# Optimization experiments

Measured on AMD Instinct MI355X. Metric: run time of the kernel, lower is better.

## Reference

```python
import jax, jax.numpy as jnp
import numpy as np

N = 100000
E = 3200000
IN_DIM = 128
HD = 64
HEADS = 4
NEG_SLOPE = 0.2


def setup_inputs() -> dict:
    key = jax.random.key(0)
    ks = jax.random.split(key, 12)
    s = lambda fan_in: 1.0 / np.sqrt(fan_in)
    x = jax.random.normal(ks[0], (N, IN_DIM), dtype=jnp.float32)
    edge_index = jax.random.randint(ks[1], (2, E), 0, N, dtype=jnp.int64)
    W1 = jax.random.normal(ks[2], (IN_DIM, HEADS * HD), dtype=jnp.float32) * s(IN_DIM)
    a_src1 = jax.random.normal(ks[3], (HEADS, HD), dtype=jnp.float32) * s(HD)
    a_dst1 = jax.random.normal(ks[4], (HEADS, HD), dtype=jnp.float32) * s(HD)
    b1 = jnp.zeros((HEADS * HD,), dtype=jnp.float32)
    W2 = jax.random.normal(ks[5], (HEADS * HD, HD), dtype=jnp.float32) * s(HEADS * HD)
    a_src2 = jax.random.normal(ks[6], (1, HD), dtype=jnp.float32) * s(HD)
    a_dst2 = jax.random.normal(ks[7], (1, HD), dtype=jnp.float32) * s(HD)
    b2 = jnp.zeros((HD,), dtype=jnp.float32)
    lin_w = jax.random.normal(ks[8], (HD, 2), dtype=jnp.float32) * s(HD)
    lin_b = jnp.zeros((2,), dtype=jnp.float32)
    return {"x": x, "edge_index": edge_index, "W1": W1, "a_src1": a_src1,
            "a_dst1": a_dst1, "b1": b1, "W2": W2, "a_src2": a_src2,
            "a_dst2": a_dst2, "b2": b2, "lin_w": lin_w, "lin_b": lin_b}


def gat_conv(x, src, dst, W, a_src, a_dst, bias, heads, out_dim, concat):
    n = x.shape[0]
    h = (x @ W).reshape(n, heads, out_dim)                 # [N,H,D]
    alpha_s = jnp.einsum('nhd,hd->nh', h, a_src)           # [N,H]
    alpha_d = jnp.einsum('nhd,hd->nh', h, a_dst)           # [N,H]
    e = alpha_s[src] + alpha_d[dst]                        # [Etot,H]
    e = jnp.where(e > 0, e, NEG_SLOPE * e)                 # leaky relu
    m = jax.ops.segment_max(e, dst, num_segments=n)        # scatter-softmax (stable)
    m = jnp.where(jnp.isfinite(m), m, 0.0)
    e = jnp.exp(e - m[dst])
    denom = jax.ops.segment_sum(e, dst, num_segments=n)
    alpha = e / denom[dst]                                 # [Etot,H]
    out = jax.ops.segment_sum(h[src] * alpha[:, :, None], dst, num_segments=n)  # [N,H,D]
    out = out.reshape(n, heads * out_dim) if concat else out.mean(axis=1)
    return out + bias


def reference(x, edge_index, W1, a_src1, a_dst1, b1, W2, a_src2, a_dst2, b2, lin_w, lin_b):
    n = x.shape[0]
    loops = jnp.arange(n, dtype=edge_index.dtype)
    src = jnp.concatenate([edge_index[0], loops])          # add self-loops (PyG default)
    dst = jnp.concatenate([edge_index[1], loops])
    h = gat_conv(x, src, dst, W1, a_src1, a_dst1, b1, HEADS, HD, True)
    h = jax.nn.elu(h)
    h = gat_conv(h, src, dst, W2, a_src2, a_dst2, b2, 1, HD, True)
    h = jax.nn.elu(h)
    return h @ lin_w + lin_b                               # [N,2]
```

## Files before the change

kernel.cpp:

```cpp
#include <hip/hip_runtime.h>
#include <hip/hip_fp16.h>
#include <math.h>

#define NN 100000
#define EE 3200000
#define ETOT (EE + NN)
#define NEG_SLOPE 0.2f
#define DMAX 96
#define CHUNK 4096
#define NB0 ((ETOT + CHUNK - 1) / CHUNK)
#define RB 391
#define CAP 16384

typedef _Float16 half8 __attribute__((ext_vector_type(8)));
typedef _Float16 half4v __attribute__((ext_vector_type(4)));
typedef float floatx4 __attribute__((ext_vector_type(4)));

__device__ __forceinline__ float wsum64(float v) {
#pragma unroll
  for (int o = 32; o; o >>= 1) v += __shfl_xor(v, o);
  return v;
}
__device__ __forceinline__ float lrelu(float v) { return v > 0.f ? v : NEG_SLOPE * v; }
__device__ __forceinline__ float elu1(float v) { return v > 0.f ? v : expm1f(v); }

__global__ void k_init(int* __restrict__ ccur) {
  ccur[threadIdx.x] = threadIdx.x * CAP;
}

__global__ __launch_bounds__(256) void k_pass1(const int* __restrict__ ei,
                                               int* __restrict__ ccur,
                                               unsigned* __restrict__ ebuf,
                                               const float* __restrict__ W1,
                                               const float* __restrict__ W2,
                                               _Float16* __restrict__ W1t,
                                               _Float16* __restrict__ W2t) {
  int b = blockIdx.x;
  if (b >= NB0) {
    int idx = (b - NB0) * 256 + threadIdx.x;
    if (idx < 32768) {
      int n = idx >> 7, k = idx & 127;
      W1t[idx] = (_Float16)W1[k * 256 + n];
    } else {
      int j = idx - 32768;
      int n = j >> 8, k = j & 255;
      W2t[j] = (_Float16)W2[k * 64 + n];
    }
    return;
  }
  __shared__ unsigned vv[CHUNK];
  __shared__ unsigned short cbv[CHUNK];
  __shared__ int h[256];
  __shared__ int cur[256];
  int t = threadIdx.x;
  h[t] = 0;
  __syncthreads();
  int base = b * CHUNK;
  int lim = base + CHUNK; if (lim > ETOT) lim = ETOT;
  int cnt = lim - base;
  for (int i = t; i < cnt; i += 256) {
    int e = base + i;
    int s, d;
    if (e < EE) { s = ei[e]; d = ei[EE + e]; } else { s = e - EE; d = s; }
    unsigned cb = (unsigned)d / (unsigned)RB;
    unsigned dloc = (unsigned)d - cb * (unsigned)RB;
    vv[i] = (dloc << 17) | (unsigned)s;
    cbv[i] = (unsigned short)cb;
    atomicAdd(&h[cb], 1);
  }
  __syncthreads();
  if (h[t]) cur[t] = atomicAdd(&ccur[t], h[t]);
  __syncthreads();
  for (int i = t; i < cnt; i += 256) {
    int cb = cbv[i];
    int pos = atomicAdd(&cur[cb], 1);
    ebuf[pos] = vv[i];
  }
}

__global__ __launch_bounds__(256) void k_pass2(const unsigned* __restrict__ ebuf,
                                               const int* __restrict__ ccur,
                                               int* __restrict__ offs,
                                               int* __restrict__ degarr,
                                               int* __restrict__ csr) {
  __shared__ unsigned ed[CAP];
  __shared__ int hist[RB];
  __shared__ int cur[RB];
  int b = blockIdx.x, t = threadIdx.x;
  int d0 = b * RB;
  int rb = NN - d0; if (rb > RB) rb = RB;
  int w0 = b * CAP;
  int cnt = ccur[b] - w0;
  if (cnt > CAP) cnt = CAP;
  for (int j = t; j < rb; j += 256) hist[j] = 0;
  __syncthreads();
  for (int i = t; i < cnt; i += 256) {
    unsigned v = ebuf[w0 + i];
    ed[i] = v;
    atomicAdd(&hist[v >> 17], 1);
  }
  __syncthreads();
  if (t == 0) {
    int run = w0;
    for (int j = 0; j < rb; ++j) { cur[j] = run; run += hist[j]; }
  }
  __syncthreads();
  for (int j = t; j < rb; j += 256) {
    offs[d0 + j] = cur[j];
    degarr[d0 + j] = hist[j];
  }
  __syncthreads();
  for (int i = t; i < cnt; i += 256) {
    unsigned v = ed[i];
    int pos = atomicAdd(&cur[v >> 17], 1);
    csr[pos] = (int)(v & 0x1FFFFu);
  }
}

__global__ __launch_bounds__(256) void k_gemm1m(const float* __restrict__ x,
                                                const _Float16* __restrict__ W1t,
                                                const float* __restrict__ a_src,
                                                const float* __restrict__ a_dst,
                                                _Float16* __restrict__ h1h,
                                                float* __restrict__ as_out,
                                                float* __restrict__ ad_out) {
  __shared__ _Float16 As[64][136];
  __shared__ _Float16 Wt[128][136];
  const int bx = blockIdx.x & 1;
  const int by = blockIdx.x >> 1;
  const int tid = threadIdx.x;
  const int row0 = by * 64;
#pragma unroll
  for (int i = 0; i < 8; ++i) {
    int idx = i * 256 + tid;
    int r = idx >> 5;
    int c4 = (idx & 31) * 4;
    int gr = row0 + r;
    float4 f = make_float4(0.f, 0.f, 0.f, 0.f);
    if (gr < NN) f = *(const float4*)(x + (size_t)gr * 128 + c4);
    half4v h; h[0] = (_Float16)f.x; h[1] = (_Float16)f.y; h[2] = (_Float16)f.z; h[3] = (_Float16)f.w;
    *(half4v*)&As[r][c4] = h;
  }
#pragma unroll
  for (int i = 0; i < 8; ++i) {
    int idx = i * 256 + tid;
    int r = idx >> 4;
    int g = idx & 15;
    *(half8*)&Wt[r][g * 8] = *(const half8*)(W1t + (size_t)(bx * 128 + r) * 128 + g * 8);
  }
  __syncthreads();

  const int wid = tid >> 6, lane = tid & 63;
  const int m16 = lane & 15, quad = lane >> 4;
  floatx4 acc[8];
#pragma unroll
  for (int nt = 0; nt < 8; ++nt) acc[nt] = (floatx4){0.f, 0.f, 0.f, 0.f};
#pragma unroll
  for (int ks = 0; ks < 4; ++ks) {
    half8 av = *(half8*)&As[wid * 16 + m16][ks * 32 + quad * 8];
#pragma unroll
    for (int nt = 0; nt < 8; ++nt) {
      half8 bv = *(half8*)&Wt[nt * 16 + m16][ks * 32 + quad * 8];
      acc[nt] = __builtin_amdgcn_mfma_f32_16x16x32_f16(av, bv, acc[nt], 0, 0, 0);
    }
  }
  float asr[8], adr[8];
#pragma unroll
  for (int nt = 0; nt < 8; ++nt) {
    asr[nt] = a_src[bx * 128 + nt * 16 + m16];
    adr[nt] = a_dst[bx * 128 + nt * 16 + m16];
  }
#pragma unroll
  for (int r = 0; r < 4; ++r) {
    int gr = row0 + wid * 16 + quad * 4 + r;
    bool ok = gr < NN;
#pragma unroll
    for (int hp = 0; hp < 2; ++hp) {
      float ps = 0.f, pd = 0.f;
#pragma unroll
      for (int j = 0; j < 4; ++j) {
        ps = fmaf(acc[hp * 4 + j][r], asr[hp * 4 + j], ps);
        pd = fmaf(acc[hp * 4 + j][r], adr[hp * 4 + j], pd);
      }
#pragma unroll
      for (int o = 1; o < 16; o <<= 1) { ps += __shfl_xor(ps, o); pd += __shfl_xor(pd, o); }
      if (ok && m16 == 0) {
        as_out[gr * 4 + bx * 2 + hp] = ps;
        ad_out[gr * 4 + bx * 2 + hp] = pd;
      }
    }
    if (ok) {
#pragma unroll
      for (int nt = 0; nt < 8; ++nt)
        h1h[(size_t)gr * 256 + bx * 128 + nt * 16 + m16] = (_Float16)acc[nt][r];
    }
  }
}

__global__ __launch_bounds__(256) void k_gemm2m(const _Float16* __restrict__ h1e,
                                                const _Float16* __restrict__ W2t,
                                                const float* __restrict__ a_src,
                                                const float* __restrict__ a_dst,
                                                _Float16* __restrict__ h2h,
                                                float* __restrict__ as_out,
                                                float* __restrict__ ad_out) {
  __shared__ _Float16 As2[64][136];
  __shared__ _Float16 Wt2[64][264];
  const int by = blockIdx.x;
  const int tid = threadIdx.x;
  const int row0 = by * 64;
#pragma unroll
  for (int i = 0; i < 8; ++i) {
    int idx = i * 256 + tid;
    int r = idx >> 5;
    int g = idx & 31;
    *(half8*)&Wt2[r][g * 8] = *(const half8*)(W2t + (size_t)r * 256 + g * 8);
  }
  const int wid = tid >> 6, lane = tid & 63;
  const int m16 = lane & 15, quad = lane >> 4;
  floatx4 acc[4];
#pragma unroll
  for (int nt = 0; nt < 4; ++nt) acc[nt] = (floatx4){0.f, 0.f, 0.f, 0.f};

  for (int kc = 0; kc < 2; ++kc) {
#pragma unroll
    for (int i = 0; i < 4; ++i) {
      int idx = i * 256 + tid;
      int r = idx >> 4;
      int g = idx & 15;
      int gr = row0 + r;
      half8 v = {0, 0, 0, 0, 0, 0, 0, 0};
      if (gr < NN) v = *(const half8*)(h1e + (size_t)gr * 256 + kc * 128 + g * 8);
      *(half8*)&As2[r][g * 8] = v;
    }
    __syncthreads();
#pragma unroll
    for (int ks = 0; ks < 4; ++ks) {
      half8 av = *(half8*)&As2[wid * 16 + m16][ks * 32 + quad * 8];
#pragma unroll
      for (int nt = 0; nt < 4; ++nt) {
        half8 bv = *(half8*)&Wt2[nt * 16 + m16][kc * 128 + ks * 32 + quad * 8];
        acc[nt] = __builtin_amdgcn_mfma_f32_16x16x32_f16(av, bv, acc[nt], 0, 0, 0);
      }
    }
    __syncthreads();
  }
  float asr[4], adr[4];
#pragma unroll
  for (int nt = 0; nt < 4; ++nt) {
    asr[nt] = a_src[nt * 16 + m16];
    adr[nt] = a_dst[nt * 16 + m16];
  }
#pragma unroll
  for (int r = 0; r < 4; ++r) {
    float ps = 0.f, pd = 0.f;
#pragma unroll
    for (int nt = 0; nt < 4; ++nt) {
      ps = fmaf(acc[nt][r], asr[nt], ps);
      pd = fmaf(acc[nt][r], adr[nt], pd);
    }
#pragma unroll
    for (int o = 1; o < 16; o <<= 1) { ps += __shfl_xor(ps, o); pd += __shfl_xor(pd, o); }
    int gr = row0 + wid * 16 + quad * 4 + r;
    if (gr < NN) {
      if (m16 == 0) { as_out[gr] = ps; ad_out[gr] = pd; }
#pragma unroll
      for (int nt = 0; nt < 4; ++nt)
        h2h[(size_t)gr * 64 + nt * 16 + m16] = (_Float16)acc[nt][r];
    }
  }
}

__global__ __launch_bounds__(256) void k_attn1(const int* __restrict__ offs,
                                               const int* __restrict__ degarr,
                                               const int* __restrict__ csr_src,
                                               const float* __restrict__ a_s,
                                               const float* __restrict__ a_d,
                                               const _Float16* __restrict__ h1h,
                                               const float* __restrict__ b1,
                                               _Float16* __restrict__ h1e) {
  __shared__ float alpha[4][DMAX][4];
  __shared__ int sidx[4][DMAX];
  const int wid = threadIdx.x >> 6;
  const int n = blockIdx.x * 4 + wid;
  const int lane = threadIdx.x & 63;
  const int beg = offs[n], deg = degarr[n];
  const float4 ad = *(const float4*)(a_d + n * 4);
  float4 sm = make_float4(0.f, 0.f, 0.f, 0.f);
  for (int d = lane; d < deg; d += 64) {
    int s = csr_src[beg + d];
    float4 as = *(const float4*)(a_s + s * 4);
    float e0 = __expf(lrelu(as.x + ad.x));
    float e1 = __expf(lrelu(as.y + ad.y));
    float e2 = __expf(lrelu(as.z + ad.z));
    float e3 = __expf(lrelu(as.w + ad.w));
    sm.x += e0; sm.y += e1; sm.z += e2; sm.w += e3;
    if (d < DMAX) {
      sidx[wid][d] = s;
      *(float4*)&alpha[wid][d][0] = make_float4(e0, e1, e2, e3);
    }
  }
  sm.x = wsum64(sm.x); sm.y = wsum64(sm.y); sm.z = wsum64(sm.z); sm.w = wsum64(sm.w);
  const float4 inv4 = make_float4(1.f / sm.x, 1.f / sm.y, 1.f / sm.z, 1.f / sm.w);
  const int dlim = deg < DMAX ? deg : DMAX;
  for (int d = lane; d < dlim; d += 64) {
    float4 a = *(float4*)&alpha[wid][d][0];
    a.x *= inv4.x; a.y *= inv4.y; a.z *= inv4.z; a.w *= inv4.w;
    *(float4*)&alpha[wid][d][0] = a;
  }
  const int half = lane >> 5;
  const int sub = lane & 31;
  const int head = sub >> 3;
  const _Float16* __restrict__ hb = h1h + sub * 8;
  float accv[8];
#pragma unroll
  for (int j = 0; j < 8; ++j) accv[j] = 0.f;
  int d = 0;
  for (; d + 8 <= dlim; d += 8) {
    int ss[4]; float ww[4];
#pragma unroll
    for (int u = 0; u < 4; ++u) {
      int idx = d + 2 * u + half;
      ss[u] = sidx[wid][idx];
      ww[u] = alpha[wid][idx][head];
    }
    half8 rr[4];
#pragma unroll
    for (int u = 0; u < 4; ++u)
      rr[u] = *(const half8*)(hb + (size_t)ss[u] * 256);
#pragma unroll
    for (int u = 0; u < 4; ++u) {
#pragma unroll
      for (int j = 0; j < 8; ++j)
        accv[j] = fmaf((float)rr[u][j], ww[u], accv[j]);
    }
  }
  for (; d + 2 <= dlim; d += 2) {
    int idx = d + half;
    int s = sidx[wid][idx];
    float w = alpha[wid][idx][head];
    half8 r = *(const half8*)(hb + (size_t)s * 256);
#pragma unroll
    for (int j = 0; j < 8; ++j) accv[j] = fmaf((float)r[j], w, accv[j]);
  }
  if (d < dlim) {
    int s = sidx[wid][d];
    float w = half ? 0.f : alpha[wid][d][head];
    half8 r = *(const half8*)(hb + (size_t)s * 256);
#pragma unroll
    for (int j = 0; j < 8; ++j) accv[j] = fmaf((float)r[j], w, accv[j]);
  }
  if (deg > DMAX) {
    const float adh = head == 0 ? ad.x : head == 1 ? ad.y : head == 2 ? ad.z : ad.w;
    const float invh = head == 0 ? inv4.x : head == 1 ? inv4.y : head == 2 ? inv4.z : inv4.w;
    if (!half) {
      for (int dd = DMAX; dd < deg; ++dd) {
        int s = csr_src[beg + dd];
        float w = __expf(lrelu(a_s[s * 4 + head] + adh)) * invh;
        half8 r = *(const half8*)(hb + (size_t)s * 256);
#pragma unroll
        for (int j = 0; j < 8; ++j) accv[j] = fmaf((float)r[j], w, accv[j]);
      }
    }
  }
#pragma unroll
  for (int j = 0; j < 8; ++j) accv[j] += __shfl_xor(accv[j], 32);
  if (!half) {
    const int c = sub * 8;
    float4 b0 = *(const float4*)(b1 + c);
    float4 b1v = *(const float4*)(b1 + c + 4);
    half8 o;
    o[0] = (_Float16)elu1(accv[0] + b0.x);
    o[1] = (_Float16)elu1(accv[1] + b0.y);
    o[2] = (_Float16)elu1(accv[2] + b0.z);
    o[3] = (_Float16)elu1(accv[3] + b0.w);
    o[4] = (_Float16)elu1(accv[4] + b1v.x);
    o[5] = (_Float16)elu1(accv[5] + b1v.y);
    o[6] = (_Float16)elu1(accv[6] + b1v.z);
    o[7] = (_Float16)elu1(accv[7] + b1v.w);
    *(half8*)(h1e + (size_t)n * 256 + c) = o;
  }
}

__global__ __launch_bounds__(256) void k_attn2(const int* __restrict__ offs,
                                               const int* __restrict__ degarr,
                                               const int* __restrict__ csr_src,
                                               const float* __restrict__ a_s,
                                               const float* __restrict__ a_d,
                                               const _Float16* __restrict__ h2h,
                                               const float* __restrict__ b2,
                                               const float* __restrict__ lin_w,
                                               const float* __restrict__ lin_b,
                                               float* __restrict__ out) {
  __shared__ float alpha2[4][DMAX];
  __shared__ int sidx2[4][DMAX];
  const int wid = threadIdx.x >> 6;
  const int n = blockIdx.x * 4 + wid;
  const int lane = threadIdx.x & 63;
  const int beg = offs[n], deg = degarr[n];
  const float adn = a_d[n];
  float sm = 0.f;
  for (int d = lane; d < deg; d += 64) {
    int s = csr_src[beg + d];
    float e = __expf(lrelu(a_s[s] + adn));
    sm += e;
    if (d < DMAX) { sidx2[wid][d] = s; alpha2[wid][d] = e; }
  }
  sm = wsum64(sm);
  const float inv = 1.f / sm;
  const int dlim = deg < DMAX ? deg : DMAX;
  for (int d = lane; d < dlim; d += 64) alpha2[wid][d] *= inv;
  const int g = lane >> 4;
  const int sub = lane & 15;
  const _Float16* __restrict__ hb = h2h + sub * 4;
  float a0 = 0.f, a1 = 0.f, a2 = 0.f, a3 = 0.f;
  int d = 0;
  for (; d + 8 <= dlim; d += 8) {
    int i0 = d + g, i1 = d + 4 + g;
    int s0 = sidx2[wid][i0], s1 = sidx2[wid][i1];
    float w0 = alpha2[wid][i0], w1 = alpha2[wid][i1];
    half4v r0 = *(const half4v*)(hb + (size_t)s0 * 64);
    half4v r1 = *(const half4v*)(hb + (size_t)s1 * 64);
    a0 = fmaf((float)r0[0], w0, a0); a1 = fmaf((float)r0[1], w0, a1);
    a2 = fmaf((float)r0[2], w0, a2); a3 = fmaf((float)r0[3], w0, a3);
    a0 = fmaf((float)r1[0], w1, a0); a1 = fmaf((float)r1[1], w1, a1);
    a2 = fmaf((float)r1[2], w1, a2); a3 = fmaf((float)r1[3], w1, a3);
  }
  if (d + 4 <= dlim) {
    int i0 = d + g;
    int s0 = sidx2[wid][i0];
    float w0 = alpha2[wid][i0];
    half4v r0 = *(const half4v*)(hb + (size_t)s0 * 64);
    a0 = fmaf((float)r0[0], w0, a0); a1 = fmaf((float)r0[1], w0, a1);
    a2 = fmaf((float)r0[2], w0, a2); a3 = fmaf((float)r0[3], w0, a3);
    d += 4;
  }
  if (d < dlim) {
    int idx = d + g;
    bool v = idx < dlim;
    int s = sidx2[wid][v ? idx : d];
    float w = v ? alpha2[wid][idx] : 0.f;
    half4v r = *(const half4v*)(hb + (size_t)s * 64);
    a0 = fmaf((float)r[0], w, a0); a1 = fmaf((float)r[1], w, a1);
    a2 = fmaf((float)r[2], w, a2); a3 = fmaf((float)r[3], w, a3);
  }
  if (deg > DMAX && g == 0) {
    for (int dd = DMAX; dd < deg; ++dd) {
      int s = csr_src[beg + dd];
      float w = __expf(lrelu(a_s[s] + adn)) * inv;
      half4v r = *(const half4v*)(hb + (size_t)s * 64);
      a0 = fmaf((float)r[0], w, a0); a1 = fmaf((float)r[1], w, a1);
      a2 = fmaf((float)r[2], w, a2); a3 = fmaf((float)r[3], w, a3);
    }
  }
  a0 += __shfl_xor(a0, 16); a1 += __shfl_xor(a1, 16);
  a2 += __shfl_xor(a2, 16); a3 += __shfl_xor(a3, 16);
  a0 += __shfl_xor(a0, 32); a1 += __shfl_xor(a1, 32);
  a2 += __shfl_xor(a2, 32); a3 += __shfl_xor(a3, 32);
  const int c = sub * 4;
  float4 bb = *(const float4*)(b2 + c);
  float o0 = elu1(a0 + bb.x);
  float o1 = elu1(a1 + bb.y);
  float o2 = elu1(a2 + bb.z);
  float o3 = elu1(a3 + bb.w);
  float4 lw0 = *(const float4*)(lin_w + c * 2);
  float4 lw1 = *(const float4*)(lin_w + c * 2 + 4);
  float p0 = o0 * lw0.x + o1 * lw0.z + o2 * lw1.x + o3 * lw1.z;
  float p1 = o0 * lw0.y + o1 * lw0.w + o2 * lw1.y + o3 * lw1.w;
  p0 = wsum64(p0) * 0.25f;
  p1 = wsum64(p1) * 0.25f;
  if (lane == 0) {
    out[n * 2 + 0] = p0 + lin_b[0];
    out[n * 2 + 1] = p1 + lin_b[1];
  }
}

extern "C" void kernel_launch(void* const* d_in, const int* in_sizes, int n_in,
                              void* d_out, int out_size, void* d_ws, size_t ws_size,
                              hipStream_t stream) {
  const float* x      = (const float*)d_in[0];
  const int*   ei     = (const int*)d_in[1];
  const float* W1     = (const float*)d_in[2];
  const float* a_src1 = (const float*)d_in[3];
  const float* a_dst1 = (const float*)d_in[4];
  const float* b1     = (const float*)d_in[5];
  const float* W2     = (const float*)d_in[6];
  const float* a_src2 = (const float*)d_in[7];
  const float* a_dst2 = (const float*)d_in[8];
  const float* b2     = (const float*)d_in[9];
  const float* lin_w  = (const float*)d_in[10];
  const float* lin_b  = (const float*)d_in[11];
  float* outp = (float*)d_out;

  char* w = (char*)d_ws;
  _Float16* h1h = (_Float16*)(w + 0);
  _Float16* h1e = (_Float16*)(w + 51200000);
  _Float16* h2h = (_Float16*)(w + 102400000);
  _Float16* W1t = (_Float16*)(w + 115200000);
  _Float16* W2t = (_Float16*)(w + 115265536);
  float*  as1 = (float*)(w + 115298304);
  float*  ad1 = (float*)(w + 116898304);
  float*  as2 = (float*)(w + 118498304);
  float*  ad2 = (float*)(w + 118898304);
  int*    offs = (int*)(w + 119298304);
  int*    degarr = (int*)(w + 119698304);
  int*    ccur = (int*)(w + 120098304);
  unsigned* ebuf = (unsigned*)(w + 120099328);
  int*    csr = (int*)(w + 136876544);

  k_init<<<1, 256, 0, stream>>>(ccur);
  k_pass1<<<NB0 + 192, 256, 0, stream>>>(ei, ccur, ebuf, W1, W2, W1t, W2t);
  k_pass2<<<256, 256, 0, stream>>>(ebuf, ccur, offs, degarr, csr);

  k_gemm1m<<<2 * 1563, 256, 0, stream>>>(x, W1t, a_src1, a_dst1, h1h, as1, ad1);
  k_attn1<<<NN / 4, 256, 0, stream>>>(offs, degarr, csr, as1, ad1, h1h, b1, h1e);

  k_gemm2m<<<1563, 256, 0, stream>>>(h1e, W2t, a_src2, a_dst2, h2h, as2, ad2);
  k_attn2<<<NN / 4, 256, 0, stream>>>(offs, degarr, csr, as2, ad2, h2h, b2, lin_w, lin_b, outp);
}
```

Baseline: 574.3 us.

## Fuse GEMM1 into edge-bucketing kernel and split layer-1 attention per head

The layer-1 GEMM is merged into the edge-bucketing kernel, with blocks partitioned by index, and W1 is transposed and cast to fp16 in shared memory inside each GEMM block instead of a separate pre-pass. The h1 features are now stored head-major ([head][N][64]) so each of four per-head attention launches gathers from a 12.8 MB slice that fits in cache better than the full 51 MB array. The cost is four passes over CSR indices and attention logits instead of one, an uncoalesced transposing shared-memory write of W1 in every GEMM block, and a larger shared-memory footprint for the fused kernel.

```diff
diff --git a/kernel.cpp b/kernel.cpp
--- a/kernel.cpp
+++ b/kernel.cpp
@@ -11,6 +11,7 @@
 #define NB0 ((ETOT + CHUNK - 1) / CHUNK)
 #define RB 391
 #define CAP 16384
+#define GEMM1B (2 * 1563)
 
 typedef _Float16 half8 __attribute__((ext_vector_type(8)));
 typedef _Float16 half4v __attribute__((ext_vector_type(4)));
@@ -28,53 +29,134 @@
   ccur[threadIdx.x] = threadIdx.x * CAP;
 }
 
-__global__ __launch_bounds__(256) void k_pass1(const int* __restrict__ ei,
+__global__ __launch_bounds__(256) void k_front(const int* __restrict__ ei,
                                                int* __restrict__ ccur,
                                                unsigned* __restrict__ ebuf,
                                                const float* __restrict__ W1,
                                                const float* __restrict__ W2,
-                                               _Float16* __restrict__ W1t,
-                                               _Float16* __restrict__ W2t) {
-  int b = blockIdx.x;
-  if (b >= NB0) {
-    int idx = (b - NB0) * 256 + threadIdx.x;
-    if (idx < 32768) {
-      int n = idx >> 7, k = idx & 127;
-      W1t[idx] = (_Float16)W1[k * 256 + n];
-    } else {
-      int j = idx - 32768;
-      int n = j >> 8, k = j & 255;
-      W2t[j] = (_Float16)W2[k * 64 + n];
+                                               _Float16* __restrict__ W2t,
+                                               const float* __restrict__ x,
+                                               const float* __restrict__ a_src,
+                                               const float* __restrict__ a_dst,
+                                               _Float16* __restrict__ h1h,
+                                               float* __restrict__ as_out,
+                                               float* __restrict__ ad_out) {
+  __shared__ __align__(16) char smem[52224];
+  const int b = blockIdx.x;
+  const int t = threadIdx.x;
+  if (b < NB0) {
+    unsigned* vv = (unsigned*)smem;
+    unsigned short* cbv = (unsigned short*)(smem + 16384);
+    int* h = (int*)(smem + 24576);
+    int* cur = (int*)(smem + 25600);
+    h[t] = 0;
+    __syncthreads();
+    int base = b * CHUNK;
+    int lim = base + CHUNK; if (lim > ETOT) lim = ETOT;
+    int cnt = lim - base;
+    for (int i = t; i < cnt; i += 256) {
+      int e = base + i;
+      int s, d;
+      if (e < EE) { s = ei[e]; d = ei[EE + e]; } else { s = e - EE; d = s; }
+      unsigned cb = (unsigned)d / (unsigned)RB;
+      unsigned dloc = (unsigned)d - cb * (unsigned)RB;
+      vv[i] = (dloc << 17) | (unsigned)s;
+      cbv[i] = (unsigned short)cb;
+      atomicAdd(&h[cb], 1);
+    }
+    __syncthreads();
+    if (h[t]) cur[t] = atomicAdd(&ccur[t], h[t]);
+    __syncthreads();
+    for (int i = t; i < cnt; i += 256) {
+      int cb = cbv[i];
+      int pos = atomicAdd(&cur[cb], 1);
+      ebuf[pos] = vv[i];
     }
     return;
   }
-  __shared__ unsigned vv[CHUNK];
-  __shared__ unsigned short cbv[CHUNK];
-  __shared__ int h[256];
-  __shared__ int cur[256];
-  int t = threadIdx.x;
-  h[t] = 0;
+  if (b < NB0 + 64) {
+    int idx = (b - NB0) * 256 + t;
+    int n = idx >> 8, k = idx & 255;
+    W2t[idx] = (_Float16)W2[k * 64 + n];
+    return;
+  }
+  const int bb = b - NB0 - 64;
+  const int bx = bb & 1;
+  const int by = bb >> 1;
+  _Float16 (*As)[136] = (_Float16(*)[136])smem;
+  _Float16 (*Wt)[136] = (_Float16(*)[136])(smem + 17408);
+  const int row0 = by * 64;
+#pragma unroll
+  for (int i = 0; i < 8; ++i) {
+    int idx = i * 256 + t;
+    int r = idx >> 5;
+    int c4 = (idx & 31) * 4;
+    int gr = row0 + r;
+    float4 f = make_float4(0.f, 0.f, 0.f, 0.f);
+    if (gr < NN) f = *(const float4*)(x + (size_t)gr * 128 + c4);
+    half4v hh; hh[0] = (_Float16)f.x; hh[1] = (_Float16)f.y; hh[2] = (_Float16)f.z; hh[3] = (_Float16)f.w;
+    *(half4v*)&As[r][c4] = hh;
+  }
+#pragma unroll
+  for (int i = 0; i < 16; ++i) {
+    int j = i * 256 + t;
+    int k = j >> 5;
+    int r4 = (j & 31) * 4;
+    float4 f = *(const float4*)(W1 + (size_t)k * 256 + bx * 128 + r4);
+    Wt[r4 + 0][k] = (_Float16)f.x;
+    Wt[r4 + 1][k] = (_Float16)f.y;
+    Wt[r4 + 2][k] = (_Float16)f.z;
+    Wt[r4 + 3][k] = (_Float16)f.w;
+  }
   __syncthreads();
-  int base = b * CHUNK;
-  int lim = base + CHUNK; if (lim > ETOT) lim = ETOT;
-  int cnt = lim - base;
-  for (int i = t; i < cnt; i += 256) {
-    int e = base + i;
-    int s, d;
-    if (e < EE) { s = ei[e]; d = ei[EE + e]; } else { s = e - EE; d = s; }
-    unsigned cb = (unsigned)d / (unsigned)RB;
-    unsigned dloc = (unsigned)d - cb * (unsigned)RB;
-    vv[i] = (dloc << 17) | (unsigned)s;
-    cbv[i] = (unsigned short)cb;
-    atomicAdd(&h[cb], 1);
-  }
-  __syncthreads();
-  if (h[t]) cur[t] = atomicAdd(&ccur[t], h[t]);
-  __syncthreads();
-  for (int i = t; i < cnt; i += 256) {
-    int cb = cbv[i];
-    int pos = atomicAdd(&cur[cb], 1);
-    ebuf[pos] = vv[i];
+
+  const int wid = t >> 6, lane = t & 63;
+  const int m16 = lane & 15, quad = lane >> 4;
+  floatx4 acc[8];
+#pragma unroll
+  for (int nt = 0; nt < 8; ++nt) acc[nt] = (floatx4){0.f, 0.f, 0.f, 0.f};
+#pragma unroll
+  for (int ks = 0; ks < 4; ++ks) {
+    half8 av = *(half8*)&As[wid * 16 + m16][ks * 32 + quad * 8];
+#pragma unroll
+    for (int nt = 0; nt < 8; ++nt) {
+      half8 bv = *(half8*)&Wt[nt * 16 + m16][ks * 32 + quad * 8];
+      acc[nt] = __builtin_amdgcn_mfma_f32_16x16x32_f16(av, bv, acc[nt], 0, 0, 0);
+    }
+  }
+  float asr[8], adr[8];
+#pragma unroll
+  for (int nt = 0; nt < 8; ++nt) {
+    asr[nt] = a_src[bx * 128 + nt * 16 + m16];
+    adr[nt] = a_dst[bx * 128 + nt * 16 + m16];
+  }
+#pragma unroll
+  for (int r = 0; r < 4; ++r) {
+    int gr = row0 + wid * 16 + quad * 4 + r;
+    bool ok = gr < NN;
+#pragma unroll
+    for (int hp = 0; hp < 2; ++hp) {
+      float ps = 0.f, pd = 0.f;
+#pragma unroll
+      for (int j = 0; j < 4; ++j) {
+        ps = fmaf(acc[hp * 4 + j][r], asr[hp * 4 + j], ps);
+        pd = fmaf(acc[hp * 4 + j][r], adr[hp * 4 + j], pd);
+      }
+#pragma unroll
+      for (int o = 1; o < 16; o <<= 1) { ps += __shfl_xor(ps, o); pd += __shfl_xor(pd, o); }
+      if (ok && m16 == 0) {
+        as_out[gr * 4 + bx * 2 + hp] = ps;
+        ad_out[gr * 4 + bx * 2 + hp] = pd;
+      }
+    }
+    if (ok) {
+#pragma unroll
+      for (int nt = 0; nt < 8; ++nt) {
+        int head = bx * 2 + (nt >> 2);
+        int dim = (nt & 3) * 16 + m16;
+        h1h[((size_t)head * NN + gr) * 64 + dim] = (_Float16)acc[nt][r];
+      }
+    }
   }
 }
 
@@ -117,83 +199,97 @@
   }
 }
 
-__global__ __launch_bounds__(256) void k_gemm1m(const float* __restrict__ x,
-                                                const _Float16* __restrict__ W1t,
-                                                const float* __restrict__ a_src,
-                                                const float* __restrict__ a_dst,
-                                                _Float16* __restrict__ h1h,
-                                                float* __restrict__ as_out,
-                                                float* __restrict__ ad_out) {
-  __shared__ _Float16 As[64][136];
-  __shared__ _Float16 Wt[128][136];
-  const int bx = blockIdx.x & 1;
-  const int by = blockIdx.x >> 1;
-  const int tid = threadIdx.x;
-  const int row0 = by * 64;
-#pragma unroll
-  for (int i = 0; i < 8; ++i) {
-    int idx = i * 256 + tid;
-    int r = idx >> 5;
-    int c4 = (idx & 31) * 4;
-    int gr = row0 + r;
-    float4 f = make_float4(0.f, 0.f, 0.f, 0.f);
-    if (gr < NN) f = *(const float4*)(x + (size_t)gr * 128 + c4);
-    half4v h; h[0] = (_Float16)f.x; h[1] = (_Float16)f.y; h[2] = (_Float16)f.z; h[3] = (_Float16)f.w;
-    *(half4v*)&As[r][c4] = h;
-  }
-#pragma unroll
-  for (int i = 0; i < 8; ++i) {
-    int idx = i * 256 + tid;
-    int r = idx >> 4;
-    int g = idx & 15;
-    *(half8*)&Wt[r][g * 8] = *(const half8*)(W1t + (size_t)(bx * 128 + r) * 128 + g * 8);
-  }
-  __syncthreads();
-
-  const int wid = tid >> 6, lane = tid & 63;
-  const int m16 = lane & 15, quad = lane >> 4;
-  floatx4 acc[8];
-#pragma unroll
-  for (int nt = 0; nt < 8; ++nt) acc[nt] = (floatx4){0.f, 0.f, 0.f, 0.f};
-#pragma unroll
-  for (int ks = 0; ks < 4; ++ks) {
-    half8 av = *(half8*)&As[wid * 16 + m16][ks * 32 + quad * 8];
-#pragma unroll
-    for (int nt = 0; nt < 8; ++nt) {
-      half8 bv = *(half8*)&Wt[nt * 16 + m16][ks * 32 + quad * 8];
-      acc[nt] = __builtin_amdgcn_mfma_f32_16x16x32_f16(av, bv, acc[nt], 0, 0, 0);
-    }
-  }
-  float asr[8], adr[8];
-#pragma unroll
-  for (int nt = 0; nt < 8; ++nt) {
-    asr[nt] = a_src[bx * 128 + nt * 16 + m16];
-    adr[nt] = a_dst[bx * 128 + nt * 16 + m16];
-  }
-#pragma unroll
-  for (int r = 0; r < 4; ++r) {
-    int gr = row0 + wid * 16 + quad * 4 + r;
-    bool ok = gr < NN;
-#pragma unroll
-    for (int hp = 0; hp < 2; ++hp) {
-      float ps = 0.f, pd = 0.f;
-#pragma unroll
-      for (int j = 0; j < 4; ++j) {
-        ps = fmaf(acc[hp * 4 + j][r], asr[hp * 4 + j], ps);
-        pd = fmaf(acc[hp * 4 + j][r], adr[hp * 4 + j], pd);
-      }
-#pragma unroll
-      for (int o = 1; o < 16; o <<= 1) { ps += __shfl_xor(ps, o); pd += __shfl_xor(pd, o); }
-      if (ok && m16 == 0) {
-        as_out[gr * 4 + bx * 2 + hp] = ps;
-        ad_out[gr * 4 + bx * 2 + hp] = pd;
-      }
-    }
-    if (ok) {
-#pragma unroll
-      for (int nt = 0; nt < 8; ++nt)
-        h1h[(size_t)gr * 256 + bx * 128 + nt * 16 + m16] = (_Float16)acc[nt][r];
-    }
+__global__ __launch_bounds__(256) void k_attn1h(const int* __restrict__ offs,
+                                                const int* __restrict__ degarr,
+                                                const int* __restrict__ csr_src,
+                                                const float* __restrict__ a_s,
+                                                const float* __restrict__ a_d,
+                                                const _Float16* __restrict__ h1h,
+                                                const float* __restrict__ b1,
+                                                _Float16* __restrict__ h1e,
+                                                int head) {
+  __shared__ float alp[4][DMAX];
+  __shared__ int sidx[4][DMAX];
+  const int wid = threadIdx.x >> 6;
+  const int n = blockIdx.x * 4 + wid;
+  const int lane = threadIdx.x & 63;
+  const int beg = offs[n], deg = degarr[n];
+  const float adh = a_d[n * 4 + head];
+  float sm = 0.f;
+  for (int d = lane; d < deg; d += 64) {
+    int s = csr_src[beg + d];
+    float e = __expf(lrelu(a_s[s * 4 + head] + adh));
+    sm += e;
+    if (d < DMAX) { sidx[wid][d] = s; alp[wid][d] = e; }
+  }
+  sm = wsum64(sm);
+  const float inv = 1.f / sm;
+  const int dlim = deg < DMAX ? deg : DMAX;
+  for (int d = lane; d < dlim; d += 64) alp[wid][d] *= inv;
+  const int g = lane >> 3;
+  const int sub = lane & 7;
+  const _Float16* __restrict__ hb = h1h + (size_t)head * NN * 64 + sub * 8;
+  float acc[8];
+#pragma unroll
+  for (int j = 0; j < 8; ++j) acc[j] = 0.f;
+  int d = 0;
+  for (; d + 32 <= dlim; d += 32) {
+    int ss[4]; float ww[4];
+#pragma unroll
+    for (int u = 0; u < 4; ++u) {
+      int idx = d + u * 8 + g;
+      ss[u] = sidx[wid][idx];
+      ww[u] = alp[wid][idx];
+    }
+    half8 rr[4];
+#pragma unroll
+    for (int u = 0; u < 4; ++u)
+      rr[u] = *(const half8*)(hb + (size_t)ss[u] * 64);
+#pragma unroll
+    for (int u = 0; u < 4; ++u) {
+#pragma unroll
+      for (int j = 0; j < 8; ++j)
+        acc[j] = fmaf((float)rr[u][j], ww[u], acc[j]);
+    }
+  }
+  for (; d + 8 <= dlim; d += 8) {
+    int idx = d + g;
+    int s = sidx[wid][idx];
+    float w = alp[wid][idx];
+    half8 r = *(const half8*)(hb + (size_t)s * 64);
+#pragma unroll
+    for (int j = 0; j < 8; ++j) acc[j] = fmaf((float)r[j], w, acc[j]);
+  }
+  if (d < dlim) {
+    int idx = d + g;
+    bool v = idx < dlim;
+    int s = sidx[wid][v ? idx : d];
+    float w = v ? alp[wid][idx] : 0.f;
+    half8 r = *(const half8*)(hb + (size_t)s * 64);
+#pragma unroll
+    for (int j = 0; j < 8; ++j) acc[j] = fmaf((float)r[j], w, acc[j]);
+  }
+  if (deg > DMAX && g == 0) {
+    for (int dd = DMAX; dd < deg; ++dd) {
+      int s = csr_src[beg + dd];
+      float w = __expf(lrelu(a_s[s * 4 + head] + adh)) * inv;
+      half8 r = *(const half8*)(hb + (size_t)s * 64);
+#pragma unroll
+      for (int j = 0; j < 8; ++j) acc[j] = fmaf((float)r[j], w, acc[j]);
+    }
+  }
+#pragma unroll
+  for (int j = 0; j < 8; ++j) {
+    acc[j] += __shfl_xor(acc[j], 8);
+    acc[j] += __shfl_xor(acc[j], 16);
+    acc[j] += __shfl_xor(acc[j], 32);
+  }
+  if (g == 0) {
+    const int c = head * 64 + sub * 8;
+    half8 o;
+#pragma unroll
+    for (int j = 0; j < 8; ++j) o[j] = (_Float16)elu1(acc[j] + b1[c + j]);
+    *(half8*)(h1e + (size_t)n * 256 + c) = o;
   }
 }
 
@@ -268,117 +364,6 @@
       for (int nt = 0; nt < 4; ++nt)
         h2h[(size_t)gr * 64 + nt * 16 + m16] = (_Float16)acc[nt][r];
     }
-  }
-}
-
-__global__ __launch_bounds__(256) void k_attn1(const int* __restrict__ offs,
-                                               const int* __restrict__ degarr,
-                                               const int* __restrict__ csr_src,
-                                               const float* __restrict__ a_s,
-                                               const float* __restrict__ a_d,
-                                               const _Float16* __restrict__ h1h,
-                                               const float* __restrict__ b1,
-                                               _Float16* __restrict__ h1e) {
-  __shared__ float alpha[4][DMAX][4];
-  __shared__ int sidx[4][DMAX];
-  const int wid = threadIdx.x >> 6;
-  const int n = blockIdx.x * 4 + wid;
-  const int lane = threadIdx.x & 63;
-  const int beg = offs[n], deg = degarr[n];
-  const float4 ad = *(const float4*)(a_d + n * 4);
-  float4 sm = make_float4(0.f, 0.f, 0.f, 0.f);
-  for (int d = lane; d < deg; d += 64) {
-    int s = csr_src[beg + d];
-    float4 as = *(const float4*)(a_s + s * 4);
-    float e0 = __expf(lrelu(as.x + ad.x));
-    float e1 = __expf(lrelu(as.y + ad.y));
-    float e2 = __expf(lrelu(as.z + ad.z));
-    float e3 = __expf(lrelu(as.w + ad.w));
-    sm.x += e0; sm.y += e1; sm.z += e2; sm.w += e3;
-    if (d < DMAX) {
-      sidx[wid][d] = s;
-      *(float4*)&alpha[wid][d][0] = make_float4(e0, e1, e2, e3);
-    }
-  }
-  sm.x = wsum64(sm.x); sm.y = wsum64(sm.y); sm.z = wsum64(sm.z); sm.w = wsum64(sm.w);
-  const float4 inv4 = make_float4(1.f / sm.x, 1.f / sm.y, 1.f / sm.z, 1.f / sm.w);
-  const int dlim = deg < DMAX ? deg : DMAX;
-  for (int d = lane; d < dlim; d += 64) {
-    float4 a = *(float4*)&alpha[wid][d][0];
-    a.x *= inv4.x; a.y *= inv4.y; a.z *= inv4.z; a.w *= inv4.w;
-    *(float4*)&alpha[wid][d][0] = a;
-  }
-  const int half = lane >> 5;
-  const int sub = lane & 31;
-  const int head = sub >> 3;
-  const _Float16* __restrict__ hb = h1h + sub * 8;
-  float accv[8];
-#pragma unroll
-  for (int j = 0; j < 8; ++j) accv[j] = 0.f;
-  int d = 0;
-  for (; d + 8 <= dlim; d += 8) {
-    int ss[4]; float ww[4];
-#pragma unroll
-    for (int u = 0; u < 4; ++u) {
-      int idx = d + 2 * u + half;
-      ss[u] = sidx[wid][idx];
-      ww[u] = alpha[wid][idx][head];
-    }
-    half8 rr[4];
-#pragma unroll
-    for (int u = 0; u < 4; ++u)
-      rr[u] = *(const half8*)(hb + (size_t)ss[u] * 256);
-#pragma unroll
-    for (int u = 0; u < 4; ++u) {
-#pragma unroll
-      for (int j = 0; j < 8; ++j)
-        accv[j] = fmaf((float)rr[u][j], ww[u], accv[j]);
-    }
-  }
-  for (; d + 2 <= dlim; d += 2) {
-    int idx = d + half;
-    int s = sidx[wid][idx];
-    float w = alpha[wid][idx][head];
-    half8 r = *(const half8*)(hb + (size_t)s * 256);
-#pragma unroll
-    for (int j = 0; j < 8; ++j) accv[j] = fmaf((float)r[j], w, accv[j]);
-  }
-  if (d < dlim) {
-    int s = sidx[wid][d];
-    float w = half ? 0.f : alpha[wid][d][head];
-    half8 r = *(const half8*)(hb + (size_t)s * 256);
-#pragma unroll
-    for (int j = 0; j < 8; ++j) accv[j] = fmaf((float)r[j], w, accv[j]);
-  }
-  if (deg > DMAX) {
-    const float adh = head == 0 ? ad.x : head == 1 ? ad.y : head == 2 ? ad.z : ad.w;
-    const float invh = head == 0 ? inv4.x : head == 1 ? inv4.y : head == 2 ? inv4.z : inv4.w;
-    if (!half) {
-      for (int dd = DMAX; dd < deg; ++dd) {
-        int s = csr_src[beg + dd];
-        float w = __expf(lrelu(a_s[s * 4 + head] + adh)) * invh;
-        half8 r = *(const half8*)(hb + (size_t)s * 256);
-#pragma unroll
-        for (int j = 0; j < 8; ++j) accv[j] = fmaf((float)r[j], w, accv[j]);
-      }
-    }
-  }
-#pragma unroll
-  for (int j = 0; j < 8; ++j) accv[j] += __shfl_xor(accv[j], 32);
-  if (!half) {
-    const int c = sub * 8;
-    float4 b0 = *(const float4*)(b1 + c);
-    float4 b1v = *(const float4*)(b1 + c + 4);
-    half8 o;
-    o[0] = (_Float16)elu1(accv[0] + b0.x);
-    o[1] = (_Float16)elu1(accv[1] + b0.y);
-    o[2] = (_Float16)elu1(accv[2] + b0.z);
-    o[3] = (_Float16)elu1(accv[3] + b0.w);
-    o[4] = (_Float16)elu1(accv[4] + b1v.x);
-    o[5] = (_Float16)elu1(accv[5] + b1v.y);
-    o[6] = (_Float16)elu1(accv[6] + b1v.z);
-    o[7] = (_Float16)elu1(accv[7] + b1v.w);
-    *(half8*)(h1e + (size_t)n * 256 + c) = o;
   }
 }
 
@@ -496,7 +481,6 @@
   _Float16* h1h = (_Float16*)(w + 0);
   _Float16* h1e = (_Float16*)(w + 51200000);
   _Float16* h2h = (_Float16*)(w + 102400000);
-  _Float16* W1t = (_Float16*)(w + 115200000);
   _Float16* W2t = (_Float16*)(w + 115265536);
   float*  as1 = (float*)(w + 115298304);
   float*  ad1 = (float*)(w + 116898304);
@@ -509,11 +493,12 @@
   int*    csr = (int*)(w + 136876544);
 
   k_init<<<1, 256, 0, stream>>>(ccur);
-  k_pass1<<<NB0 + 192, 256, 0, stream>>>(ei, ccur, ebuf, W1, W2, W1t, W2t);
+  k_front<<<NB0 + 64 + GEMM1B, 256, 0, stream>>>(ei, ccur, ebuf, W1, W2, W2t,
+                                                 x, a_src1, a_dst1, h1h, as1, ad1);
   k_pass2<<<256, 256, 0, stream>>>(ebuf, ccur, offs, degarr, csr);
 
-  k_gemm1m<<<2 * 1563, 256, 0, stream>>>(x, W1t, a_src1, a_dst1, h1h, as1, ad1);
-  k_attn1<<<NN / 4, 256, 0, stream>>>(offs, degarr, csr, as1, ad1, h1h, b1, h1e);
+  for (int h = 0; h < 4; ++h)
+    k_attn1h<<<NN / 4, 256, 0, stream>>>(offs, degarr, csr, as1, ad1, h1h, b1, h1e, h);
 
   k_gemm2m<<<1563, 256, 0, stream>>>(h1e, W2t, a_src2, a_dst2, h2h, as2, ad2);
   k_attn2<<<NN / 4, 256, 0, stream>>>(offs, degarr, csr, as2, ad2, h2h, b2, lin_w, lin_b, outp);
```

Result: slower. 709.6 us (+23.6%).
